# Performance work log

Hardware: AMD Instinct MI355X
Metric: run time of the kernel (lower is better)

Reference implementation:

```python
import jax, jax.numpy as jnp
import numpy as np

N_NODES = 200000
N_ETYPES = 4
N_EDGES = 500000
D_IN = 128
D_OUT = 128


def setup_inputs() -> dict:
    key = jax.random.key(0)
    ks = jax.random.split(key, 7)
    scale = 1.0 / np.sqrt(D_IN)
    x = jax.random.normal(ks[0], (N_NODES, D_IN), dtype=jnp.float32)
    W = jax.random.normal(ks[1], (N_ETYPES, D_IN, D_OUT), dtype=jnp.float32) * scale
    b = jax.random.normal(ks[2], (N_ETYPES, D_OUT), dtype=jnp.float32) * 0.01
    W_self = jax.random.normal(ks[3], (D_IN, D_OUT), dtype=jnp.float32) * scale
    b_self = jax.random.normal(ks[4], (D_OUT,), dtype=jnp.float32) * 0.01
    src = jax.random.randint(ks[5], (N_ETYPES, N_EDGES), 0, N_NODES, dtype=jnp.int32)
    dst = jax.random.randint(ks[6], (N_ETYPES, N_EDGES), 0, N_NODES, dtype=jnp.int32)
    return {"x": x, "W": W, "b": b, "W_self": W_self, "b_self": b_self,
            "src": src, "dst": dst}


def _etype_mean_agg(Wx_e, src_e, dst_e, n_nodes):
    # gather transformed src features along edges, mean-reduce per dst node
    m = Wx_e[src_e]  # [E, d_out]
    s = jax.ops.segment_sum(m, dst_e, num_segments=n_nodes)  # [N, d_out]
    cnt = jax.ops.segment_sum(jnp.ones((src_e.shape[0],), dtype=Wx_e.dtype),
                              dst_e, num_segments=n_nodes)  # [N]
    # nodes with no in-edges of this etype contribute 0 (DGL leaves h unset -> 0)
    return jnp.where(cnt[:, None] > 0, s / jnp.maximum(cnt[:, None], 1.0), 0.0)


def reference(x, W, b, W_self, b_self, src, dst):
    n_nodes = x.shape[0]
    # per-etype linear transform of all node features: [T, N, d_out]
    Wx = jnp.einsum('nd,tdf->tnf', x, W) + b[:, None, :]
    # per-etype gather + segment mean, then sum across etypes ('sum' cross-reducer)
    h = jax.vmap(_etype_mean_agg, in_axes=(0, 0, 0, None))(Wx, src, dst, n_nodes)
    h = h.sum(axis=0)  # [N, d_out]
    self_msg = x @ W_self + b_self
    return self_msg + h
```

## Files before the change

### kernel.cpp

```cpp
#include <hip/hip_runtime.h>
#include <hip/hip_bf16.h>


namespace {

constexpr int N  = 200000;
constexpr int T  = 4;
constexpr int E  = 500000;
constexpr int D  = 128;
constexpr int NT = 64;
constexpr int AS = 136;

constexpr int CNT_B = (T * E + 255) / 256;
constexpr int PX_B  = (N * D / 8) / 256;
constexpr int PW_B  = (5 * D * D / 8 + 255) / 256;

typedef __bf16 bf16x8 __attribute__((ext_vector_type(8)));
typedef float  f32x4  __attribute__((ext_vector_type(4)));

__global__ void k_zero(int* __restrict__ p, int n) {
  int i = blockIdx.x * 256 + threadIdx.x;
  if (i < n) p[i] = 0;
}

template <bool XB>
__global__ void k_prep(const int* __restrict__ dst, int* __restrict__ cnt,
                       int* __restrict__ rank, const float* __restrict__ x,
                       __bf16* __restrict__ xb, const float* __restrict__ W,
                       const float* __restrict__ Wself, __bf16* __restrict__ wt) {
  const int bid = blockIdx.x;
  const int tid = threadIdx.x;
  if (bid < CNT_B) {
    int i = bid * 256 + tid;
    if (i < T * E) {
      int t = i / E;
      rank[i] = atomicAdd(&cnt[t * N + dst[i]], 1);
    }
  } else if (XB && bid < CNT_B + PX_B) {
    int i = (bid - CNT_B) * 256 + tid;
    if (i < N * D / 8) {
      const float4* xs = (const float4*)(x + i * 8);
      float4 a = xs[0], c = xs[1];
      bf16x8 v;
      v[0] = (__bf16)a.x; v[1] = (__bf16)a.y; v[2] = (__bf16)a.z; v[3] = (__bf16)a.w;
      v[4] = (__bf16)c.x; v[5] = (__bf16)c.y; v[6] = (__bf16)c.z; v[7] = (__bf16)c.w;
      *(bf16x8*)(xb + i * 8) = v;
    }
  } else {
    int i = (bid - CNT_B - (XB ? PX_B : 0)) * 256 + tid;
    if (i < 5 * D * D / 8) {
      int base = i * 8;
      int p = base >> 14, rem = base & 16383;
      int n = rem >> 7, k0 = rem & 127;
      const float* Wsrc = (p < 4) ? (W + (size_t)p * D * D) : Wself;
      bf16x8 v;
#pragma unroll
      for (int j = 0; j < 8; ++j) v[j] = (__bf16)Wsrc[(k0 + j) * D + n];
      *(bf16x8*)(wt + base) = v;
    }
  }
}

__global__ void k_offsets(const int* __restrict__ cnt, int* __restrict__ offs,
                          int* __restrict__ cursor) {
  __shared__ int s[256];
  __shared__ int base;
  int tid = threadIdx.x;
  int i = blockIdx.x * 256 + tid;
  int c = (i < T * N) ? cnt[i] : 0;
  s[tid] = c;
  __syncthreads();
  for (int d = 1; d < 256; d <<= 1) {
    int v = (tid >= d) ? s[tid - d] : 0;
    __syncthreads();
    s[tid] += v;
    __syncthreads();
  }
  if (tid == 255) base = atomicAdd(cursor, s[255]);
  __syncthreads();
  if (i < T * N) offs[i] = base + s[tid] - c;
}

__global__ void k_scatter(const int* __restrict__ src, const int* __restrict__ dst,
                          const int* __restrict__ offs, const int* __restrict__ rank,
                          int* __restrict__ eid) {
  int i = blockIdx.x * 256 + threadIdx.x;
  if (i >= T * E) return;
  int t = i / E;
  int pos = offs[t * N + dst[i]] + rank[i];
  eid[pos] = src[i];
}

template <bool XB>
__global__ __launch_bounds__(256, 3) void k_fused(
    const float* __restrict__ x, const __bf16* __restrict__ xb,
    const __bf16* __restrict__ wt, const float* __restrict__ b,
    const float* __restrict__ bself, const int* __restrict__ cnt,
    const int* __restrict__ offs, const int* __restrict__ eid,
    float* __restrict__ out) {
  __shared__ __align__(16) __bf16 a_s[NT * AS];
  __shared__ __align__(16) __bf16 w_s[D * AS];

  const int tid  = threadIdx.x;
  const int nb   = blockIdx.x * NT;
  const int wv   = tid >> 6;
  const int lane = tid & 63;
  const int quad = lane >> 4;
  const int l16  = lane & 15;
  const int ln   = tid >> 2;
  const int q    = tid & 3;

  f32x4 acc[8];
#pragma unroll
  for (int ct = 0; ct < 8; ++ct) acc[ct] = (f32x4){0.f, 0.f, 0.f, 0.f};

  for (int pass = 0; pass < 5; ++pass) {
    const bool self = (pass == 4);

    {
      const __bf16* wsrc = wt + pass * D * D;
#pragma unroll
      for (int c = 0; c < 8; ++c) {
        int idx  = c * 256 + tid;
        int row  = idx >> 4;
        int col8 = (idx & 15) * 8;
        *(bf16x8*)(w_s + row * AS + col8) = *(const bf16x8*)(wsrc + row * D + col8);
      }
    }

    if (!(XB && self)) {
      float r[32];
#pragma unroll
      for (int i = 0; i < 32; ++i) r[i] = 0.f;
      const int node = nb + ln;
      if (self) {
        const float4* xr = (const float4*)(x + node * D + q * 32);
#pragma unroll
        for (int i = 0; i < 8; ++i) {
          float4 v = xr[i];
          r[4 * i] = v.x; r[4 * i + 1] = v.y; r[4 * i + 2] = v.z; r[4 * i + 3] = v.w;
        }
      } else {
        const int base = offs[pass * N + node];
        const int deg  = cnt[pass * N + node];
        int nxt = (deg > 0) ? eid[base] : 0;
        for (int e = 0; e < deg; ++e) {
          const int sidx = nxt;
          nxt = eid[base + e + 1];
          if (XB) {
            const bf16x8* xr = (const bf16x8*)(xb + sidx * D + q * 32);
            bf16x8 v0 = xr[0], v1 = xr[1], v2 = xr[2], v3 = xr[3];
#pragma unroll
            for (int j = 0; j < 8; ++j) {
              r[j]      += (float)v0[j];
              r[8 + j]  += (float)v1[j];
              r[16 + j] += (float)v2[j];
              r[24 + j] += (float)v3[j];
            }
          } else {
            const float4* xr = (const float4*)(x + sidx * D + q * 32);
#pragma unroll
            for (int i = 0; i < 8; ++i) {
              float4 v = xr[i];
              r[4 * i] += v.x; r[4 * i + 1] += v.y;
              r[4 * i + 2] += v.z; r[4 * i + 3] += v.w;
            }
          }
        }
        const float inv = (deg > 0) ? (1.0f / (float)deg) : 0.0f;
#pragma unroll
        for (int i = 0; i < 32; ++i) r[i] *= inv;
      }
      __bf16* arow = a_s + ln * AS + q * 32;
#pragma unroll
      for (int g = 0; g < 4; ++g) {
        bf16x8 v;
#pragma unroll
        for (int j = 0; j < 8; ++j) v[j] = (__bf16)r[8 * g + j];
        *(bf16x8*)(arow + g * 8) = v;
      }
    }
    __syncthreads();

#pragma unroll
    for (int ks = 0; ks < 4; ++ks) {
      bf16x8 af;
      if (XB && self) {
        af = *(const bf16x8*)(xb + (nb + 16 * wv + l16) * D + ks * 32 + quad * 8);
      } else {
        af = *(const bf16x8*)(a_s + (16 * wv + l16) * AS + ks * 32 + quad * 8);
      }
#pragma unroll
      for (int ct = 0; ct < 8; ++ct) {
        bf16x8 bfr = *(const bf16x8*)(w_s + (16 * ct + l16) * AS + ks * 32 + quad * 8);
        acc[ct] = __builtin_amdgcn_mfma_f32_16x16x32_bf16(af, bfr, acc[ct], 0, 0, 0);
      }
    }

    {
      const float* bt = self ? bself : (b + pass * D);
      bool rowon[4];
#pragma unroll
      for (int r = 0; r < 4; ++r) {
        rowon[r] = self ? true : (cnt[pass * N + nb + 16 * wv + quad * 4 + r] > 0);
      }
#pragma unroll
      for (int ct = 0; ct < 8; ++ct) {
        float bv = bt[16 * ct + l16];
#pragma unroll
        for (int r = 0; r < 4; ++r)
          if (rowon[r]) acc[ct][r] += bv;
      }
    }
    if (pass < 4) __syncthreads();
  }

#pragma unroll
  for (int ct = 0; ct < 8; ++ct) {
#pragma unroll
    for (int r = 0; r < 4; ++r) {
      out[(nb + 16 * wv + quad * 4 + r) * D + 16 * ct + l16] = acc[ct][r];
    }
  }
}

}

extern "C" void kernel_launch(void* const* d_in, const int* in_sizes, int n_in,
                              void* d_out, int out_size, void* d_ws, size_t ws_size,
                              hipStream_t stream) {
  const float* x     = (const float*)d_in[0];
  const float* W     = (const float*)d_in[1];
  const float* b     = (const float*)d_in[2];
  const float* Wself = (const float*)d_in[3];
  const float* bself = (const float*)d_in[4];
  const int*   src   = (const int*)d_in[5];
  const int*   dst   = (const int*)d_in[6];
  float* out = (float*)d_out;

  int* cnt    = (int*)d_ws;
  int* cursor = cnt + T * N;
  int* offs   = cursor + 4;
  int* eid    = offs + T * N;
  int* rank   = eid + T * E;
  __bf16* wt  = (__bf16*)(rank + T * E);
  __bf16* xb  = wt + 5 * D * D;

  const size_t need_xb =
      (size_t)(T * N + 4 + T * N + T * E + T * E) * 4 + (size_t)5 * D * D * 2 +
      (size_t)N * D * 2;
  const bool use_xb = ws_size >= need_xb;

  k_zero<<<(T * N + 4 + 255) / 256, 256, 0, stream>>>(cnt, T * N + 4);
  if (use_xb) {
    k_prep<true><<<CNT_B + PX_B + PW_B, 256, 0, stream>>>(dst, cnt, rank, x, xb,
                                                          W, Wself, wt);
  } else {
    k_prep<false><<<CNT_B + PW_B, 256, 0, stream>>>(dst, cnt, rank, x, xb, W,
                                                    Wself, wt);
  }
  k_offsets<<<(T * N + 255) / 256, 256, 0, stream>>>(cnt, offs, cursor);
  k_scatter<<<(T * E + 255) / 256, 256, 0, stream>>>(src, dst, offs, rank, eid);
  if (use_xb) {
    k_fused<true><<<N / NT, 256, 0, stream>>>(x, xb, wt, b, bself, cnt, offs,
                                              eid, out);
  } else {
    k_fused<false><<<N / NT, 256, 0, stream>>>(x, xb, wt, b, bself, cnt, offs,
                                               eid, out);
  }
}
```

Measured before the change: 546.1 us.

## Gather aggregated rows directly into MFMA fragments, drop shared memory staging

Each lane now gathers and averages the exact source-row slice it needs as its MFMA A operand, so the aggregated features never pass through shared memory. Weight B-fragments are read straight from global memory (expected to hit cache) instead of being staged in LDS, which removes all __syncthreads. The occupancy hint rises from 3 to 5 blocks. The trade-off is that gather work is now split across 16-byte per-lane chunks with four lanes sharing a node, and the weights are re-read from global/L2 by every wave.

```diff
diff --git a/kernel.cpp b/kernel.cpp
--- a/kernel.cpp
+++ b/kernel.cpp
@@ -9,7 +9,6 @@
 constexpr int E  = 500000;
 constexpr int D  = 128;
 constexpr int NT = 64;
-constexpr int AS = 136;
 
 constexpr int CNT_B = (T * E + 255) / 256;
 constexpr int PX_B  = (N * D / 8) / 256;
@@ -92,23 +91,19 @@
 }
 
 template <bool XB>
-__global__ __launch_bounds__(256, 3) void k_fused(
+__global__ __launch_bounds__(256, 5) void k_fused(
     const float* __restrict__ x, const __bf16* __restrict__ xb,
     const __bf16* __restrict__ wt, const float* __restrict__ b,
     const float* __restrict__ bself, const int* __restrict__ cnt,
     const int* __restrict__ offs, const int* __restrict__ eid,
     float* __restrict__ out) {
-  __shared__ __align__(16) __bf16 a_s[NT * AS];
-  __shared__ __align__(16) __bf16 w_s[D * AS];
-
   const int tid  = threadIdx.x;
   const int nb   = blockIdx.x * NT;
   const int wv   = tid >> 6;
   const int lane = tid & 63;
   const int quad = lane >> 4;
   const int l16  = lane & 15;
-  const int ln   = tid >> 2;
-  const int q    = tid & 3;
+  const int node = nb + 16 * wv + l16;
 
   f32x4 acc[8];
 #pragma unroll
@@ -117,83 +112,73 @@
   for (int pass = 0; pass < 5; ++pass) {
     const bool self = (pass == 4);
 
-    {
-      const __bf16* wsrc = wt + pass * D * D;
-#pragma unroll
-      for (int c = 0; c < 8; ++c) {
-        int idx  = c * 256 + tid;
-        int row  = idx >> 4;
-        int col8 = (idx & 15) * 8;
-        *(bf16x8*)(w_s + row * AS + col8) = *(const bf16x8*)(wsrc + row * D + col8);
-      }
-    }
-
-    if (!(XB && self)) {
-      float r[32];
-#pragma unroll
-      for (int i = 0; i < 32; ++i) r[i] = 0.f;
-      const int node = nb + ln;
-      if (self) {
-        const float4* xr = (const float4*)(x + node * D + q * 32);
-#pragma unroll
-        for (int i = 0; i < 8; ++i) {
-          float4 v = xr[i];
-          r[4 * i] = v.x; r[4 * i + 1] = v.y; r[4 * i + 2] = v.z; r[4 * i + 3] = v.w;
+    bf16x8 af[4];
+    if (self) {
+      if (XB) {
+#pragma unroll
+        for (int ks = 0; ks < 4; ++ks)
+          af[ks] = *(const bf16x8*)(xb + (size_t)node * D + ks * 32 + quad * 8);
+      } else {
+#pragma unroll
+        for (int ks = 0; ks < 4; ++ks) {
+          const float* xr = x + (size_t)node * D + ks * 32 + quad * 8;
+          float4 a = *(const float4*)xr;
+          float4 c = *(const float4*)(xr + 4);
+          bf16x8 v;
+          v[0] = (__bf16)a.x; v[1] = (__bf16)a.y; v[2] = (__bf16)a.z; v[3] = (__bf16)a.w;
+          v[4] = (__bf16)c.x; v[5] = (__bf16)c.y; v[6] = (__bf16)c.z; v[7] = (__bf16)c.w;
+          af[ks] = v;
         }
-      } else {
-        const int base = offs[pass * N + node];
-        const int deg  = cnt[pass * N + node];
-        int nxt = (deg > 0) ? eid[base] : 0;
-        for (int e = 0; e < deg; ++e) {
-          const int sidx = nxt;
-          nxt = eid[base + e + 1];
-          if (XB) {
-            const bf16x8* xr = (const bf16x8*)(xb + sidx * D + q * 32);
-            bf16x8 v0 = xr[0], v1 = xr[1], v2 = xr[2], v3 = xr[3];
-#pragma unroll
-            for (int j = 0; j < 8; ++j) {
-              r[j]      += (float)v0[j];
-              r[8 + j]  += (float)v1[j];
-              r[16 + j] += (float)v2[j];
-              r[24 + j] += (float)v3[j];
-            }
-          } else {
-            const float4* xr = (const float4*)(x + sidx * D + q * 32);
-#pragma unroll
-            for (int i = 0; i < 8; ++i) {
-              float4 v = xr[i];
-              r[4 * i] += v.x; r[4 * i + 1] += v.y;
-              r[4 * i + 2] += v.z; r[4 * i + 3] += v.w;
-            }
+      }
+    } else {
+      float r[4][8];
+#pragma unroll
+      for (int ks = 0; ks < 4; ++ks)
+#pragma unroll
+        for (int j = 0; j < 8; ++j) r[ks][j] = 0.f;
+
+      const int bucket = pass * N + node;
+      const int base = offs[bucket];
+      const int deg  = cnt[bucket];
+      int nxt = (deg > 0) ? eid[base] : 0;
+      for (int e = 0; e < deg; ++e) {
+        const int sidx = nxt;
+        nxt = eid[base + e + 1];
+        if (XB) {
+#pragma unroll
+          for (int ks = 0; ks < 4; ++ks) {
+            bf16x8 v = *(const bf16x8*)(xb + (size_t)sidx * D + ks * 32 + quad * 8);
+#pragma unroll
+            for (int j = 0; j < 8; ++j) r[ks][j] += (float)v[j];
+          }
+        } else {
+#pragma unroll
+          for (int ks = 0; ks < 4; ++ks) {
+            const float* xr = x + (size_t)sidx * D + ks * 32 + quad * 8;
+            float4 a = *(const float4*)xr;
+            float4 c = *(const float4*)(xr + 4);
+            r[ks][0] += a.x; r[ks][1] += a.y; r[ks][2] += a.z; r[ks][3] += a.w;
+            r[ks][4] += c.x; r[ks][5] += c.y; r[ks][6] += c.z; r[ks][7] += c.w;
           }
         }
-        const float inv = (deg > 0) ? (1.0f / (float)deg) : 0.0f;
-#pragma unroll
-        for (int i = 0; i < 32; ++i) r[i] *= inv;
-      }
-      __bf16* arow = a_s + ln * AS + q * 32;
-#pragma unroll
-      for (int g = 0; g < 4; ++g) {
+      }
+      const float inv = (deg > 0) ? (1.0f / (float)deg) : 0.0f;
+#pragma unroll
+      for (int ks = 0; ks < 4; ++ks) {
         bf16x8 v;
 #pragma unroll
-        for (int j = 0; j < 8; ++j) v[j] = (__bf16)r[8 * g + j];
-        *(bf16x8*)(arow + g * 8) = v;
-      }
-    }
-    __syncthreads();
-
+        for (int j = 0; j < 8; ++j) v[j] = (__bf16)(r[ks][j] * inv);
+        af[ks] = v;
+      }
+    }
+
+    const __bf16* wp = wt + pass * D * D;
 #pragma unroll
     for (int ks = 0; ks < 4; ++ks) {
-      bf16x8 af;
-      if (XB && self) {
-        af = *(const bf16x8*)(xb + (nb + 16 * wv + l16) * D + ks * 32 + quad * 8);
-      } else {
-        af = *(const bf16x8*)(a_s + (16 * wv + l16) * AS + ks * 32 + quad * 8);
-      }
 #pragma unroll
       for (int ct = 0; ct < 8; ++ct) {
-        bf16x8 bfr = *(const bf16x8*)(w_s + (16 * ct + l16) * AS + ks * 32 + quad * 8);
-        acc[ct] = __builtin_amdgcn_mfma_f32_16x16x32_bf16(af, bfr, acc[ct], 0, 0, 0);
+        bf16x8 bfr = *(const bf16x8*)(wp + (16 * ct + l16) * D + ks * 32 + quad * 8);
+        acc[ct] = __builtin_amdgcn_mfma_f32_16x16x32_bf16(af[ks], bfr, acc[ct], 0, 0, 0);
       }
     }
 
@@ -212,7 +197,6 @@
           if (rowon[r]) acc[ct][r] += bv;
       }
     }
-    if (pass < 4) __syncthreads();
   }
 
 #pragma unroll
```

Result: slower. 729.1 us (+33.5%).
